# Optimization experiments

Hardware: AMD Instinct MI355X
Metric: run time of the kernel (lower is better)

The kernel has to match this reference:

```python
import jax, jax.numpy as jnp
import numpy as np

N, D, E, K = 16384, 512, 8, 2  # tokens, model dim, experts, top_k


def setup_inputs() -> dict:
    key = jax.random.key(0)
    k_x, k_l, k_w = jax.random.split(key, 3)
    input_batch = jax.random.normal(k_x, (N, D), dtype=jnp.float32)
    # Router-like top-k gates: distinct expert ids per token (matches the
    # module's assumption that each (token, slot) maps to a unique expert row).
    logits = jax.random.normal(k_l, (N, E), dtype=jnp.float32)
    top_vals, top_idx = jax.lax.top_k(logits, K)
    probabilities = jax.nn.softmax(top_vals, axis=-1)          # [N, K]
    indices = top_idx.astype(jnp.int32)                        # [N, K]
    W = jax.random.normal(k_w, (E, D, D), dtype=jnp.float32) * (1.0 / np.sqrt(D))
    b = jnp.zeros((E, D), dtype=jnp.float32)
    return {"input_batch": input_batch, "probabilities": probabilities,
            "indices": indices, "W": W, "b": b}


def reference(input_batch, probabilities, indices, W, b):
    # Original loops over experts, gathers tokens routed to each expert,
    # runs the expert, concatenates, restores original (token, slot) order,
    # applies AFTER_EXPERTS gate weighting, and sums over the top_k slots.
    # Equivalent vectorized math: out[n] = sum_k p[n,k] * expert_{idx[n,k]}(x[n]).
    y = jnp.einsum('nd,edo->eno', input_batch, W) + b[:, None, :]   # [E, N, D]
    n_ar = jnp.arange(input_batch.shape[0])[:, None]                # [N, 1]
    gathered = y[indices, n_ar]                                     # [N, K, D]
    output = jnp.sum(probabilities[..., None] * gathered, axis=1)   # [N, D]
    total_loss = jnp.float32(0.0)  # sampler_loss=0 (external indices), expert losses=0
    return output, total_loss
```

## Files before the change

### kernel.cpp

```cpp
#include <hip/hip_runtime.h>

#define NTOK 16384
#define DIM  512
#define NEXP 8
#define NPAIR 64
#define PCAP 8192

#define BM 128
#define BN 64
#define BK 32

typedef __bf16 bf16x8 __attribute__((ext_vector_type(8)));
typedef __bf16 bf16x4 __attribute__((ext_vector_type(4)));
typedef float  f32x4  __attribute__((ext_vector_type(4)));

__device__ __forceinline__ void async_cp16(const void* g, void* l) {
    __builtin_amdgcn_global_load_lds((const __attribute__((address_space(1))) void*)g,
                                     (__attribute__((address_space(3))) void*)l, 16, 0, 0);
}

__global__ __launch_bounds__(256) void k_prep(const float* __restrict__ W,
                                              __bf16* __restrict__ Wt,
                                              const float* __restrict__ x,
                                              __bf16* __restrict__ xb,
                                              const int* __restrict__ indices,
                                              const float* __restrict__ probs,
                                              int* __restrict__ cnt,
                                              int* __restrict__ tok_arr,
                                              float* __restrict__ plo_arr,
                                              float* __restrict__ phi_arr,
                                              float* __restrict__ out) {
    int b = blockIdx.x, tid = threadIdx.x;
    if (b < 512) {
        __shared__ __bf16 tile[64][66];
        int e = b >> 6, rem = b & 63;
        int o0 = (rem >> 3) * 64, k0 = (rem & 7) * 64;
        const float* Wsrc = W + ((size_t)e * DIM + k0) * DIM + o0;
        for (int i = tid; i < 4096; i += 256) {
            int kk = i >> 6, oo = i & 63;
            tile[oo][kk] = (__bf16)Wsrc[(size_t)kk * DIM + oo];
        }
        __syncthreads();
        for (int i = tid; i < 512; i += 256) {
            int oo = i >> 3, kk8 = (i & 7) * 8;
            int kg = k0 + kk8;
            __bf16* dst = Wt + ((size_t)(e * 16 + (kg >> 5)) * DIM + o0 + oo) * 32 + (kg & 31);
            bf16x8 v;
            #pragma unroll
            for (int j = 0; j < 8; ++j) v[j] = tile[oo][kk8 + j];
            *(bf16x8*)dst = v;
        }
    } else if (b < 1536) {
        int c = b - 512;
        const float4* src = (const float4*)x;
        #pragma unroll
        for (int it = 0; it < 4; ++it) {
            int pi = c * 1024 + it * 256 + tid;
            float4 v0 = src[2 * pi], v1 = src[2 * pi + 1];
            bf16x8 h;
            h[0] = (__bf16)v0.x; h[1] = (__bf16)v0.y; h[2] = (__bf16)v0.z; h[3] = (__bf16)v0.w;
            h[4] = (__bf16)v1.x; h[5] = (__bf16)v1.y; h[6] = (__bf16)v1.z; h[7] = (__bf16)v1.w;
            *(bf16x8*)&xb[(size_t)pi * 8] = h;
        }
    } else {
        __shared__ int lcnt[NPAIR], lbase[NPAIR];
        int t = (b - 1536) * 256 + tid;
        if (tid < NPAIR) lcnt[tid] = 0;
        __syncthreads();
        int   e0 = indices[2 * t], e1 = indices[2 * t + 1];
        float p0 = probs[2 * t],   p1 = probs[2 * t + 1];
        int lo = min(e0, e1), hi = max(e0, e1);
        float plo = (e0 < e1) ? p0 : p1;
        float phi = (e0 < e1) ? p1 : p0;
        int key = lo * 8 + hi;
        int lr = atomicAdd(&lcnt[key], 1);
        __syncthreads();
        if (tid < NPAIR) lbase[tid] = atomicAdd(&cnt[tid], lcnt[tid]);
        __syncthreads();
        int pos = lbase[key] + lr;
        if (pos < PCAP) {
            int q = key * PCAP + pos;
            tok_arr[q] = t; plo_arr[q] = plo; phi_arr[q] = phi;
        }
        if (b == 1536 && tid == 0) out[NTOK * DIM] = 0.0f;
    }
}

__global__ __launch_bounds__(256, 3) void k_gemm(const __bf16* __restrict__ xb,
                                                 const __bf16* __restrict__ Wt,
                                                 const float* __restrict__ bias,
                                                 const int* __restrict__ tok_arr,
                                                 const float* __restrict__ plo_arr,
                                                 const float* __restrict__ phi_arr,
                                                 const int* __restrict__ cnt,
                                                 float* __restrict__ out) {
    int p = blockIdx.x;
    int r = p & 7;
    int nt = (p >> 3) & 7;
    int m_slot = (p >> 6) * 8 + r;
    int key = -1, m_t = 0, count = 0, total = 0;
    for (int i = 0; i < NPAIR; ++i) {
        int c = cnt[i];
        int tl = (c + BM - 1) >> 7;
        if (key < 0 && m_slot < total + tl) { key = i; m_t = m_slot - total; count = c; }
        total += tl;
    }
    if (key < 0) return;
    if (count > PCAP) count = PCAP;
    int lo = key >> 3, hi = key & 7;
    int m0 = m_t * BM, n0 = nt * BN, tid = threadIdx.x;

    __shared__ __attribute__((aligned(16))) char smem[49152];
    __shared__ int   sTok[BM];
    __shared__ float sPlo[BM], sPhi[BM];

    if (tid < BM) {
        int g = m0 + tid;
        int tk = 0; float a = 0.f, h = 0.f;
        if (g < count) {
            int q = key * PCAP + g;
            tk = tok_arr[q]; a = plo_arr[q]; h = phi_arr[q];
        }
        sTok[tid] = tk;
        sPlo[tid] = a; sPhi[tid] = h;
    }
    __syncthreads();

    int wid  = tid >> 6, lane = tid & 63;
    int quad = lane >> 4, rr  = lane & 15;
    int wm = (wid >> 1) * 64, wn = (wid & 1) * 32;

    int rA0 = tid >> 2;
    int swz = ((tid & 3) ^ ((rA0 >> 1) & 3)) << 3;
    const __bf16* gA0 = xb + (size_t)sTok[rA0]      * DIM + swz;
    const __bf16* gA1 = xb + (size_t)sTok[rA0 + 64] * DIM + swz;
    size_t bOff = (size_t)((rA0 * 4 + ((tid & 3) ^ ((rA0 >> 1) & 3))) * 8);
    const __bf16* gBlo = Wt + ((size_t)(lo * 16) * DIM + n0) * 32 + bOff;
    const __bf16* gBhi = Wt + ((size_t)(hi * 16) * DIM + n0) * 32 + bOff;

    f32x4 accL[4][2] = {};
    f32x4 accH[4][2] = {};

    auto issue = [&](int kt, int b) {
        int ka = kt * BK;
        size_t wOff = (size_t)kt * DIM * 32;
        async_cp16(gA0 + ka,    smem + b * 8192 + tid * 16);
        async_cp16(gA1 + ka,    smem + b * 8192 + tid * 16 + 4096);
        async_cp16(gBlo + wOff, smem + 24576 + b * 4096 + tid * 16);
        async_cp16(gBhi + wOff, smem + 36864 + b * 4096 + tid * 16);
    };

    issue(0, 0);
    issue(1, 1);

    int cur = 0;
    #pragma unroll
    for (int kt = 0; kt < 16; ++kt) {
        if (kt < 15) { asm volatile("s_waitcnt vmcnt(4)" ::: "memory"); }
        else         { asm volatile("s_waitcnt vmcnt(0)" ::: "memory"); }
        __builtin_amdgcn_s_barrier();
        asm volatile("" ::: "memory");
        if (kt < 14) issue(kt + 2, cur == 0 ? 2 : cur - 1);

        const __bf16* sA  = (const __bf16*)(smem +         cur * 8192);
        const __bf16* sBl = (const __bf16*)(smem + 24576 + cur * 4096);
        const __bf16* sBh = (const __bf16*)(smem + 36864 + cur * 4096);
        int csw = (quad ^ ((rr >> 1) & 3)) * 8;
        bf16x8 af[4], bl[2], bh[2];
        #pragma unroll
        for (int i = 0; i < 4; ++i)
            af[i] = *(bf16x8*)&sA[(wm + i * 16 + rr) * BK + csw];
        #pragma unroll
        for (int j = 0; j < 2; ++j) {
            bl[j] = *(bf16x8*)&sBl[(wn + j * 16 + rr) * BK + csw];
            bh[j] = *(bf16x8*)&sBh[(wn + j * 16 + rr) * BK + csw];
        }
        __builtin_amdgcn_s_setprio(1);
        #pragma unroll
        for (int i = 0; i < 4; ++i)
            #pragma unroll
            for (int j = 0; j < 2; ++j) {
                accL[i][j] = __builtin_amdgcn_mfma_f32_16x16x32_bf16(af[i], bl[j], accL[i][j], 0, 0, 0);
                accH[i][j] = __builtin_amdgcn_mfma_f32_16x16x32_bf16(af[i], bh[j], accH[i][j], 0, 0, 0);
            }
        __builtin_amdgcn_s_setprio(0);
        cur = (cur == 2) ? 0 : cur + 1;
    }

    float blo[2], bhi[2];
    #pragma unroll
    for (int j = 0; j < 2; ++j) {
        blo[j] = bias[lo * DIM + n0 + wn + j * 16 + rr];
        bhi[j] = bias[hi * DIM + n0 + wn + j * 16 + rr];
    }
    #pragma unroll
    for (int i = 0; i < 4; ++i) {
        #pragma unroll
        for (int reg = 0; reg < 4; ++reg) {
            int row = wm + i * 16 + quad * 4 + reg;
            int g = m0 + row;
            if (g >= count) continue;
            int   tk = sTok[row];
            float pl = sPlo[row], ph = sPhi[row];
            float* dst = out + (size_t)tk * DIM + n0 + wn + rr;
            #pragma unroll
            for (int j = 0; j < 2; ++j)
                dst[j * 16] = accL[i][j][reg] * pl + accH[i][j][reg] * ph + pl * blo[j] + ph * bhi[j];
        }
    }
}

extern "C" void kernel_launch(void* const* d_in, const int* in_sizes, int n_in,
                              void* d_out, int out_size, void* d_ws, size_t ws_size,
                              hipStream_t stream) {
    const float* x    = (const float*)d_in[0];
    const float* prob = (const float*)d_in[1];
    const int*   idx  = (const int*)d_in[2];
    const float* W    = (const float*)d_in[3];
    const float* b    = (const float*)d_in[4];
    float* out = (float*)d_out;

    char* ws = (char*)d_ws;
    __bf16* Wt      = (__bf16*)ws;
    __bf16* xb      = (__bf16*)(ws + 4194304);
    int*    cnt     = (int*)   (ws + 4194304 + 16777216);
    int*    tok_arr = (int*)   (ws + 4194304 + 16777216 + 256);
    float*  plo_arr = (float*) (ws + 4194304 + 16777216 + 256 + 2097152);
    float*  phi_arr = (float*) (ws + 4194304 + 16777216 + 256 + 2 * 2097152);

    (void)hipMemsetAsync(cnt, 0, NPAIR * sizeof(int), stream);
    hipLaunchKernelGGL(k_prep, dim3(1600), dim3(256), 0, stream,
                       W, Wt, x, xb, idx, prob, cnt, tok_arr, plo_arr, phi_arr, out);
    hipLaunchKernelGGL(k_gemm, dim3(1280), dim3(256), 0, stream,
                       xb, Wt, b, tok_arr, plo_arr, phi_arr, cnt, out);
}
```

Measured before the change: 130.6 us.

## Load expert weight fragments directly into registers and shrink LDS pipeline

The weight (B) operand now skips LDS: each lane loads its MFMA fragment straight from global memory into registers, prefetched one K-step ahead. Only the gathered token rows (A) still go through LDS, now with two buffers instead of three, synchronised by a plain barrier instead of hand-written vmcnt waits. This cuts LDS from 48KB to 16KB per block to allow more resident blocks and removes LDS traffic for B. In exchange, B loads are no longer shared across waves, global load latency is exposed through registers, and prefetch depth drops from two stages to one.

```diff
diff --git a/kernel.cpp b/kernel.cpp
--- a/kernel.cpp
+++ b/kernel.cpp
@@ -110,7 +110,7 @@
     int lo = key >> 3, hi = key & 7;
     int m0 = m_t * BM, n0 = nt * BN, tid = threadIdx.x;
 
-    __shared__ __attribute__((aligned(16))) char smem[49152];
+    __shared__ __attribute__((aligned(16))) char smem[16384];
     __shared__ int   sTok[BM];
     __shared__ float sPlo[BM], sPhi[BM];
 
@@ -134,57 +134,54 @@
     int swz = ((tid & 3) ^ ((rA0 >> 1) & 3)) << 3;
     const __bf16* gA0 = xb + (size_t)sTok[rA0]      * DIM + swz;
     const __bf16* gA1 = xb + (size_t)sTok[rA0 + 64] * DIM + swz;
-    size_t bOff = (size_t)((rA0 * 4 + ((tid & 3) ^ ((rA0 >> 1) & 3))) * 8);
-    const __bf16* gBlo = Wt + ((size_t)(lo * 16) * DIM + n0) * 32 + bOff;
-    const __bf16* gBhi = Wt + ((size_t)(hi * 16) * DIM + n0) * 32 + bOff;
+
+    const __bf16* pBlo = Wt + ((size_t)(lo * 16) * DIM + n0 + wn + rr) * 32 + quad * 8;
+    const __bf16* pBhi = Wt + ((size_t)(hi * 16) * DIM + n0 + wn + rr) * 32 + quad * 8;
 
     f32x4 accL[4][2] = {};
     f32x4 accH[4][2] = {};
 
-    auto issue = [&](int kt, int b) {
+    auto issueA = [&](int kt, int b) {
         int ka = kt * BK;
-        size_t wOff = (size_t)kt * DIM * 32;
-        async_cp16(gA0 + ka,    smem + b * 8192 + tid * 16);
-        async_cp16(gA1 + ka,    smem + b * 8192 + tid * 16 + 4096);
-        async_cp16(gBlo + wOff, smem + 24576 + b * 4096 + tid * 16);
-        async_cp16(gBhi + wOff, smem + 36864 + b * 4096 + tid * 16);
+        async_cp16(gA0 + ka, smem + b * 8192 + tid * 16);
+        async_cp16(gA1 + ka, smem + b * 8192 + tid * 16 + 4096);
     };
 
-    issue(0, 0);
-    issue(1, 1);
-
-    int cur = 0;
+    issueA(0, 0);
+    bf16x8 cbl0 = *(const bf16x8*)(pBlo);
+    bf16x8 cbl1 = *(const bf16x8*)(pBlo + 16 * 32);
+    bf16x8 cbh0 = *(const bf16x8*)(pBhi);
+    bf16x8 cbh1 = *(const bf16x8*)(pBhi + 16 * 32);
+
     #pragma unroll
     for (int kt = 0; kt < 16; ++kt) {
-        if (kt < 15) { asm volatile("s_waitcnt vmcnt(4)" ::: "memory"); }
-        else         { asm volatile("s_waitcnt vmcnt(0)" ::: "memory"); }
-        __builtin_amdgcn_s_barrier();
-        asm volatile("" ::: "memory");
-        if (kt < 14) issue(kt + 2, cur == 0 ? 2 : cur - 1);
-
-        const __bf16* sA  = (const __bf16*)(smem +         cur * 8192);
-        const __bf16* sBl = (const __bf16*)(smem + 24576 + cur * 4096);
-        const __bf16* sBh = (const __bf16*)(smem + 36864 + cur * 4096);
+        int cur = kt & 1;
+        __syncthreads();
+        bf16x8 nbl0, nbl1, nbh0, nbh1;
+        if (kt < 15) {
+            issueA(kt + 1, cur ^ 1);
+            size_t wOff = (size_t)(kt + 1) * DIM * 32;
+            nbl0 = *(const bf16x8*)(pBlo + wOff);
+            nbl1 = *(const bf16x8*)(pBlo + wOff + 16 * 32);
+            nbh0 = *(const bf16x8*)(pBhi + wOff);
+            nbh1 = *(const bf16x8*)(pBhi + wOff + 16 * 32);
+        }
+        const __bf16* sA = (const __bf16*)(smem + cur * 8192);
         int csw = (quad ^ ((rr >> 1) & 3)) * 8;
-        bf16x8 af[4], bl[2], bh[2];
+        bf16x8 af[4];
         #pragma unroll
         for (int i = 0; i < 4; ++i)
             af[i] = *(bf16x8*)&sA[(wm + i * 16 + rr) * BK + csw];
-        #pragma unroll
-        for (int j = 0; j < 2; ++j) {
-            bl[j] = *(bf16x8*)&sBl[(wn + j * 16 + rr) * BK + csw];
-            bh[j] = *(bf16x8*)&sBh[(wn + j * 16 + rr) * BK + csw];
-        }
         __builtin_amdgcn_s_setprio(1);
         #pragma unroll
-        for (int i = 0; i < 4; ++i)
-            #pragma unroll
-            for (int j = 0; j < 2; ++j) {
-                accL[i][j] = __builtin_amdgcn_mfma_f32_16x16x32_bf16(af[i], bl[j], accL[i][j], 0, 0, 0);
-                accH[i][j] = __builtin_amdgcn_mfma_f32_16x16x32_bf16(af[i], bh[j], accH[i][j], 0, 0, 0);
-            }
+        for (int i = 0; i < 4; ++i) {
+            accL[i][0] = __builtin_amdgcn_mfma_f32_16x16x32_bf16(af[i], cbl0, accL[i][0], 0, 0, 0);
+            accL[i][1] = __builtin_amdgcn_mfma_f32_16x16x32_bf16(af[i], cbl1, accL[i][1], 0, 0, 0);
+            accH[i][0] = __builtin_amdgcn_mfma_f32_16x16x32_bf16(af[i], cbh0, accH[i][0], 0, 0, 0);
+            accH[i][1] = __builtin_amdgcn_mfma_f32_16x16x32_bf16(af[i], cbh1, accH[i][1], 0, 0, 0);
+        }
         __builtin_amdgcn_s_setprio(0);
-        cur = (cur == 2) ? 0 : cur + 1;
+        if (kt < 15) { cbl0 = nbl0; cbl1 = nbl1; cbh0 = nbh0; cbh1 = nbh1; }
     }
 
     float blo[2], bhi[2];
```

After: 137.7 us. +5.5%, slower.

## Route first, then scatter bf16 activations into per-pair contiguous layout for GEMM

Applied to the files above, without the earlier changes.

Routing moves into its own kernel that also records each token's slot. The conversion kernel then writes bf16 rows of x directly into an expert-pair-sorted buffer, so GEMM A-tile loads read contiguous rows instead of gathering through token indices. PCAP drops to 2048 and overflowing tokens are clamped onto the last slot, which could corrupt results if a pair holds more than 2048 tokens. It adds a kernel launch and a serial dependency between routing and conversion.

```diff
diff --git a/kernel.cpp b/kernel.cpp
--- a/kernel.cpp
+++ b/kernel.cpp
@@ -4,14 +4,13 @@
 #define DIM  512
 #define NEXP 8
 #define NPAIR 64
-#define PCAP 8192
+#define PCAP 2048
 
 #define BM 128
 #define BN 64
 #define BK 32
 
 typedef __bf16 bf16x8 __attribute__((ext_vector_type(8)));
-typedef __bf16 bf16x4 __attribute__((ext_vector_type(4)));
 typedef float  f32x4  __attribute__((ext_vector_type(4)));
 
 __device__ __forceinline__ void async_cp16(const void* g, void* l) {
@@ -19,17 +18,41 @@
                                      (__attribute__((address_space(3))) void*)l, 16, 0, 0);
 }
 
+__global__ __launch_bounds__(256) void k_route(const int* __restrict__ indices,
+                                               const float* __restrict__ probs,
+                                               int* __restrict__ cnt,
+                                               int* __restrict__ tok_arr,
+                                               float* __restrict__ plo_arr,
+                                               float* __restrict__ phi_arr,
+                                               int* __restrict__ pos_arr,
+                                               float* __restrict__ out) {
+    __shared__ int lcnt[NPAIR], lbase[NPAIR];
+    int b = blockIdx.x, tid = threadIdx.x;
+    int t = b * 256 + tid;
+    if (tid < NPAIR) lcnt[tid] = 0;
+    __syncthreads();
+    int   e0 = indices[2 * t], e1 = indices[2 * t + 1];
+    float p0 = probs[2 * t],   p1 = probs[2 * t + 1];
+    int lo = min(e0, e1), hi = max(e0, e1);
+    float plo = (e0 < e1) ? p0 : p1;
+    float phi = (e0 < e1) ? p1 : p0;
+    int key = (lo * 8 + hi) & 63;
+    int lr = atomicAdd(&lcnt[key], 1);
+    __syncthreads();
+    if (tid < NPAIR) lbase[tid] = atomicAdd(&cnt[tid], lcnt[tid]);
+    __syncthreads();
+    int pos = lbase[key] + lr;
+    int q = key * PCAP + min(pos, PCAP - 1);
+    tok_arr[q] = t; plo_arr[q] = plo; phi_arr[q] = phi;
+    pos_arr[t] = q;
+    if (b == 0 && tid == 0) out[NTOK * DIM] = 0.0f;
+}
+
 __global__ __launch_bounds__(256) void k_prep(const float* __restrict__ W,
                                               __bf16* __restrict__ Wt,
                                               const float* __restrict__ x,
-                                              __bf16* __restrict__ xb,
-                                              const int* __restrict__ indices,
-                                              const float* __restrict__ probs,
-                                              int* __restrict__ cnt,
-                                              int* __restrict__ tok_arr,
-                                              float* __restrict__ plo_arr,
-                                              float* __restrict__ phi_arr,
-                                              float* __restrict__ out) {
+                                              __bf16* __restrict__ xs,
+                                              const int* __restrict__ pos_arr) {
     int b = blockIdx.x, tid = threadIdx.x;
     if (b < 512) {
         __shared__ __bf16 tile[64][66];
@@ -50,43 +73,26 @@
             for (int j = 0; j < 8; ++j) v[j] = tile[oo][kk8 + j];
             *(bf16x8*)dst = v;
         }
-    } else if (b < 1536) {
+    } else {
         int c = b - 512;
-        const float4* src = (const float4*)x;
+        int t0 = c * 16;
         #pragma unroll
         for (int it = 0; it < 4; ++it) {
-            int pi = c * 1024 + it * 256 + tid;
-            float4 v0 = src[2 * pi], v1 = src[2 * pi + 1];
+            int i = it * 256 + tid;
+            int row = i >> 6, ch = i & 63;
+            int t = t0 + row;
+            int q = pos_arr[t];
+            const float4* src = (const float4*)(x + (size_t)t * DIM) + ch * 2;
+            float4 v0 = src[0], v1 = src[1];
             bf16x8 h;
             h[0] = (__bf16)v0.x; h[1] = (__bf16)v0.y; h[2] = (__bf16)v0.z; h[3] = (__bf16)v0.w;
             h[4] = (__bf16)v1.x; h[5] = (__bf16)v1.y; h[6] = (__bf16)v1.z; h[7] = (__bf16)v1.w;
-            *(bf16x8*)&xb[(size_t)pi * 8] = h;
-        }
-    } else {
-        __shared__ int lcnt[NPAIR], lbase[NPAIR];
-        int t = (b - 1536) * 256 + tid;
-        if (tid < NPAIR) lcnt[tid] = 0;
-        __syncthreads();
-        int   e0 = indices[2 * t], e1 = indices[2 * t + 1];
-        float p0 = probs[2 * t],   p1 = probs[2 * t + 1];
-        int lo = min(e0, e1), hi = max(e0, e1);
-        float plo = (e0 < e1) ? p0 : p1;
-        float phi = (e0 < e1) ? p1 : p0;
-        int key = lo * 8 + hi;
-        int lr = atomicAdd(&lcnt[key], 1);
-        __syncthreads();
-        if (tid < NPAIR) lbase[tid] = atomicAdd(&cnt[tid], lcnt[tid]);
-        __syncthreads();
-        int pos = lbase[key] + lr;
-        if (pos < PCAP) {
-            int q = key * PCAP + pos;
-            tok_arr[q] = t; plo_arr[q] = plo; phi_arr[q] = phi;
-        }
-        if (b == 1536 && tid == 0) out[NTOK * DIM] = 0.0f;
-    }
-}
-
-__global__ __launch_bounds__(256, 3) void k_gemm(const __bf16* __restrict__ xb,
+            *(bf16x8*)&xs[(size_t)q * DIM + ch * 8] = h;
+        }
+    }
+}
+
+__global__ __launch_bounds__(256, 3) void k_gemm(const __bf16* __restrict__ xs,
                                                  const __bf16* __restrict__ Wt,
                                                  const float* __restrict__ bias,
                                                  const int* __restrict__ tok_arr,
@@ -132,8 +138,8 @@
 
     int rA0 = tid >> 2;
     int swz = ((tid & 3) ^ ((rA0 >> 1) & 3)) << 3;
-    const __bf16* gA0 = xb + (size_t)sTok[rA0]      * DIM + swz;
-    const __bf16* gA1 = xb + (size_t)sTok[rA0 + 64] * DIM + swz;
+    const __bf16* gA0 = xs + ((size_t)(key * PCAP + m0 + rA0)) * DIM + swz;
+    const __bf16* gA1 = gA0 + (size_t)64 * DIM;
     size_t bOff = (size_t)((rA0 * 4 + ((tid & 3) ^ ((rA0 >> 1) & 3))) * 8);
     const __bf16* gBlo = Wt + ((size_t)(lo * 16) * DIM + n0) * 32 + bOff;
     const __bf16* gBhi = Wt + ((size_t)(hi * 16) * DIM + n0) * 32 + bOff;
@@ -222,15 +228,18 @@
 
     char* ws = (char*)d_ws;
     __bf16* Wt      = (__bf16*)ws;
-    __bf16* xb      = (__bf16*)(ws + 4194304);
-    int*    cnt     = (int*)   (ws + 4194304 + 16777216);
-    int*    tok_arr = (int*)   (ws + 4194304 + 16777216 + 256);
-    float*  plo_arr = (float*) (ws + 4194304 + 16777216 + 256 + 2097152);
-    float*  phi_arr = (float*) (ws + 4194304 + 16777216 + 256 + 2 * 2097152);
+    __bf16* xs      = (__bf16*)(ws + 4194304);
+    int*    cnt     = (int*)   (ws + 138412032);
+    int*    tok_arr = (int*)   (ws + 138412288);
+    float*  plo_arr = (float*) (ws + 138936576);
+    float*  phi_arr = (float*) (ws + 139460864);
+    int*    pos_arr = (int*)   (ws + 139985152);
 
     (void)hipMemsetAsync(cnt, 0, NPAIR * sizeof(int), stream);
-    hipLaunchKernelGGL(k_prep, dim3(1600), dim3(256), 0, stream,
-                       W, Wt, x, xb, idx, prob, cnt, tok_arr, plo_arr, phi_arr, out);
+    hipLaunchKernelGGL(k_route, dim3(64), dim3(256), 0, stream,
+                       idx, prob, cnt, tok_arr, plo_arr, phi_arr, pos_arr, out);
+    hipLaunchKernelGGL(k_prep, dim3(1536), dim3(256), 0, stream,
+                       W, Wt, x, xs, pos_arr);
     hipLaunchKernelGGL(k_gemm, dim3(1280), dim3(256), 0, stream,
-                       xb, Wt, b, tok_arr, plo_arr, phi_arr, cnt, out);
-}
+                       xs, Wt, b, tok_arr, plo_arr, phi_arr, cnt, out);
+}
```

New measurement: 132.9 us. Within noise of the previous version (+1.8%).

## Fuse fp32-to-bf16 conversion of activations into the expert GEMM A-tile load

Applied to the files above, without the earlier changes.

Removes the separate pass that converted the whole input to bf16 in the prep kernel; the GEMM now async-copies fp32 token rows into shared memory with an XOR swizzle and converts to bf16 when building MFMA fragments. This removes a full read/write sweep over the activations and the bf16 workspace. In exchange A-tile loads and LDS footprint double, and the pipeline shrinks from triple to double buffering with a full barrier each step, which may expose more load latency.

```diff
diff --git a/kernel.cpp b/kernel.cpp
--- a/kernel.cpp
+++ b/kernel.cpp
@@ -11,7 +11,6 @@
 #define BK 32
 
 typedef __bf16 bf16x8 __attribute__((ext_vector_type(8)));
-typedef __bf16 bf16x4 __attribute__((ext_vector_type(4)));
 typedef float  f32x4  __attribute__((ext_vector_type(4)));
 
 __device__ __forceinline__ void async_cp16(const void* g, void* l) {
@@ -21,8 +20,6 @@
 
 __global__ __launch_bounds__(256) void k_prep(const float* __restrict__ W,
                                               __bf16* __restrict__ Wt,
-                                              const float* __restrict__ x,
-                                              __bf16* __restrict__ xb,
                                               const int* __restrict__ indices,
                                               const float* __restrict__ probs,
                                               int* __restrict__ cnt,
@@ -50,21 +47,9 @@
             for (int j = 0; j < 8; ++j) v[j] = tile[oo][kk8 + j];
             *(bf16x8*)dst = v;
         }
-    } else if (b < 1536) {
-        int c = b - 512;
-        const float4* src = (const float4*)x;
-        #pragma unroll
-        for (int it = 0; it < 4; ++it) {
-            int pi = c * 1024 + it * 256 + tid;
-            float4 v0 = src[2 * pi], v1 = src[2 * pi + 1];
-            bf16x8 h;
-            h[0] = (__bf16)v0.x; h[1] = (__bf16)v0.y; h[2] = (__bf16)v0.z; h[3] = (__bf16)v0.w;
-            h[4] = (__bf16)v1.x; h[5] = (__bf16)v1.y; h[6] = (__bf16)v1.z; h[7] = (__bf16)v1.w;
-            *(bf16x8*)&xb[(size_t)pi * 8] = h;
-        }
     } else {
         __shared__ int lcnt[NPAIR], lbase[NPAIR];
-        int t = (b - 1536) * 256 + tid;
+        int t = (b - 512) * 256 + tid;
         if (tid < NPAIR) lcnt[tid] = 0;
         __syncthreads();
         int   e0 = indices[2 * t], e1 = indices[2 * t + 1];
@@ -82,11 +67,11 @@
             int q = key * PCAP + pos;
             tok_arr[q] = t; plo_arr[q] = plo; phi_arr[q] = phi;
         }
-        if (b == 1536 && tid == 0) out[NTOK * DIM] = 0.0f;
-    }
-}
-
-__global__ __launch_bounds__(256, 3) void k_gemm(const __bf16* __restrict__ xb,
+        if (b == 512 && tid == 0) out[NTOK * DIM] = 0.0f;
+    }
+}
+
+__global__ __launch_bounds__(256, 3) void k_gemm(const float* __restrict__ x,
                                                  const __bf16* __restrict__ Wt,
                                                  const float* __restrict__ bias,
                                                  const int* __restrict__ tok_arr,
@@ -130,11 +115,14 @@
     int quad = lane >> 4, rr  = lane & 15;
     int wm = (wid >> 1) * 64, wn = (wid & 1) * 32;
 
-    int rA0 = tid >> 2;
-    int swz = ((tid & 3) ^ ((rA0 >> 1) & 3)) << 3;
-    const __bf16* gA0 = xb + (size_t)sTok[rA0]      * DIM + swz;
-    const __bf16* gA1 = xb + (size_t)sTok[rA0 + 64] * DIM + swz;
-    size_t bOff = (size_t)((rA0 * 4 + ((tid & 3) ^ ((rA0 >> 1) & 3))) * 8);
+    int rowA = tid >> 3, cpos = tid & 7;
+    int srcCh = (cpos ^ (rowA & 7)) * 4;
+    const float* gA0 = x + (size_t)sTok[rowA]      * DIM + srcCh;
+    const float* gA1 = x + (size_t)sTok[rowA + 32] * DIM + srcCh;
+    const float* gA2 = x + (size_t)sTok[rowA + 64] * DIM + srcCh;
+    const float* gA3 = x + (size_t)sTok[rowA + 96] * DIM + srcCh;
+    int rB = tid >> 2;
+    size_t bOff = (size_t)((rB * 4 + ((tid & 3) ^ ((rB >> 1) & 3))) * 8);
     const __bf16* gBlo = Wt + ((size_t)(lo * 16) * DIM + n0) * 32 + bOff;
     const __bf16* gBhi = Wt + ((size_t)(hi * 16) * DIM + n0) * 32 + bOff;
 
@@ -144,32 +132,40 @@
     auto issue = [&](int kt, int b) {
         int ka = kt * BK;
         size_t wOff = (size_t)kt * DIM * 32;
-        async_cp16(gA0 + ka,    smem + b * 8192 + tid * 16);
-        async_cp16(gA1 + ka,    smem + b * 8192 + tid * 16 + 4096);
-        async_cp16(gBlo + wOff, smem + 24576 + b * 4096 + tid * 16);
-        async_cp16(gBhi + wOff, smem + 36864 + b * 4096 + tid * 16);
+        char* aBase = smem + b * 16384 + tid * 16;
+        async_cp16(gA0 + ka,    aBase);
+        async_cp16(gA1 + ka,    aBase + 4096);
+        async_cp16(gA2 + ka,    aBase + 8192);
+        async_cp16(gA3 + ka,    aBase + 12288);
+        async_cp16(gBlo + wOff, smem + 32768 + b * 4096 + tid * 16);
+        async_cp16(gBhi + wOff, smem + 40960 + b * 4096 + tid * 16);
     };
 
     issue(0, 0);
-    issue(1, 1);
-
-    int cur = 0;
-    #pragma unroll
+
+    #pragma unroll 2
     for (int kt = 0; kt < 16; ++kt) {
-        if (kt < 15) { asm volatile("s_waitcnt vmcnt(4)" ::: "memory"); }
-        else         { asm volatile("s_waitcnt vmcnt(0)" ::: "memory"); }
-        __builtin_amdgcn_s_barrier();
-        asm volatile("" ::: "memory");
-        if (kt < 14) issue(kt + 2, cur == 0 ? 2 : cur - 1);
-
-        const __bf16* sA  = (const __bf16*)(smem +         cur * 8192);
-        const __bf16* sBl = (const __bf16*)(smem + 24576 + cur * 4096);
-        const __bf16* sBh = (const __bf16*)(smem + 36864 + cur * 4096);
+        int cur = kt & 1;
+        __syncthreads();
+        if (kt < 15) issue(kt + 1, cur ^ 1);
+
+        const float*  sA  = (const float*)(smem + cur * 16384);
+        const __bf16* sBl = (const __bf16*)(smem + 32768 + cur * 4096);
+        const __bf16* sBh = (const __bf16*)(smem + 40960 + cur * 4096);
         int csw = (quad ^ ((rr >> 1) & 3)) * 8;
         bf16x8 af[4], bl[2], bh[2];
         #pragma unroll
-        for (int i = 0; i < 4; ++i)
-            af[i] = *(bf16x8*)&sA[(wm + i * 16 + rr) * BK + csw];
+        for (int i = 0; i < 4; ++i) {
+            int R = wm + i * 16 + rr;
+            int p0 = ((quad * 2)     ^ (R & 7)) * 4;
+            int p1 = ((quad * 2 + 1) ^ (R & 7)) * 4;
+            f32x4 a0 = *(const f32x4*)&sA[R * 32 + p0];
+            f32x4 a1 = *(const f32x4*)&sA[R * 32 + p1];
+            bf16x8 h;
+            h[0] = (__bf16)a0[0]; h[1] = (__bf16)a0[1]; h[2] = (__bf16)a0[2]; h[3] = (__bf16)a0[3];
+            h[4] = (__bf16)a1[0]; h[5] = (__bf16)a1[1]; h[6] = (__bf16)a1[2]; h[7] = (__bf16)a1[3];
+            af[i] = h;
+        }
         #pragma unroll
         for (int j = 0; j < 2; ++j) {
             bl[j] = *(bf16x8*)&sBl[(wn + j * 16 + rr) * BK + csw];
@@ -184,7 +180,6 @@
                 accH[i][j] = __builtin_amdgcn_mfma_f32_16x16x32_bf16(af[i], bh[j], accH[i][j], 0, 0, 0);
             }
         __builtin_amdgcn_s_setprio(0);
-        cur = (cur == 2) ? 0 : cur + 1;
     }
 
     float blo[2], bhi[2];
@@ -222,15 +217,14 @@
 
     char* ws = (char*)d_ws;
     __bf16* Wt      = (__bf16*)ws;
-    __bf16* xb      = (__bf16*)(ws + 4194304);
-    int*    cnt     = (int*)   (ws + 4194304 + 16777216);
-    int*    tok_arr = (int*)   (ws + 4194304 + 16777216 + 256);
-    float*  plo_arr = (float*) (ws + 4194304 + 16777216 + 256 + 2097152);
-    float*  phi_arr = (float*) (ws + 4194304 + 16777216 + 256 + 2 * 2097152);
+    int*    cnt     = (int*)   (ws + 4194304);
+    int*    tok_arr = (int*)   (ws + 4194304 + 256);
+    float*  plo_arr = (float*) (ws + 4194304 + 256 + 2097152);
+    float*  phi_arr = (float*) (ws + 4194304 + 256 + 2 * 2097152);
 
     (void)hipMemsetAsync(cnt, 0, NPAIR * sizeof(int), stream);
-    hipLaunchKernelGGL(k_prep, dim3(1600), dim3(256), 0, stream,
-                       W, Wt, x, xb, idx, prob, cnt, tok_arr, plo_arr, phi_arr, out);
+    hipLaunchKernelGGL(k_prep, dim3(576), dim3(256), 0, stream,
+                       W, Wt, idx, prob, cnt, tok_arr, plo_arr, phi_arr, out);
     hipLaunchKernelGGL(k_gemm, dim3(1280), dim3(256), 0, stream,
-                       xb, Wt, b, tok_arr, plo_arr, phi_arr, cnt, out);
-}
+                       x, Wt, b, tok_arr, plo_arr, phi_arr, cnt, out);
+}
```

After: 142.7 us. 1.09x slower.
